# Kernel optimization log

Hardware: AMD Instinct MI355X
Metric: run time of the kernel (lower is better)

The kernel has to match this reference:

```python
import jax, jax.numpy as jnp
import numpy as np

B, S, DIM, H, DH, FF = 2, 2048, 2048, 16, 128, 8192
EPS = 1e-6


def rmsnorm(x, g):
    xf = x.astype(jnp.float32)
    y = xf * jax.lax.rsqrt(jnp.mean(xf * xf, axis=-1, keepdims=True) + EPS)
    return y.astype(x.dtype) * g


def rope_cache(seq_len, head_dim):
    inv_freq = 1.0 / (10000.0 ** (jnp.arange(0, head_dim, 2, dtype=jnp.float32) / head_dim))
    t = jnp.arange(seq_len, dtype=jnp.float32)
    freqs = jnp.outer(t, inv_freq)              # [S, DH/2]
    emb = jnp.concatenate([freqs, freqs], -1)   # [S, DH]
    return jnp.cos(emb), jnp.sin(emb)


def rotate_half(x):
    x1, x2 = jnp.split(x, 2, axis=-1)
    return jnp.concatenate([-x2, x1], axis=-1)


def apply_rope(x, cos, sin):
    # x: [B,H,S,DH]; cos/sin: [S,DH] broadcast per position
    c = cos[None, None, :, :]
    s = sin[None, None, :, :]
    return x * c + rotate_half(x) * s


def setup_inputs() -> dict:
    key = jax.random.key(0)
    ks = jax.random.split(key, 10)
    std = 0.02
    x = jax.random.normal(ks[0], (B, S, DIM), jnp.float32)
    mask = jnp.tril(jnp.ones((S, S), dtype=bool))[None, None]  # causal [1,1,S,S]
    wq = jax.random.normal(ks[1], (H * DH, DIM), jnp.float32) * std
    wk = jax.random.normal(ks[2], (H * DH, DIM), jnp.float32) * std
    wv = jax.random.normal(ks[3], (H * DH, DIM), jnp.float32) * std
    wo = jax.random.normal(ks[4], (DIM, H * DH), jnp.float32) * std
    w1 = jax.random.normal(ks[5], (FF, DIM), jnp.float32) * std
    w2 = jax.random.normal(ks[6], (DIM, FF), jnp.float32) * std
    w3 = jax.random.normal(ks[7], (FF, DIM), jnp.float32) * std
    g_attn = jnp.ones((DIM,), jnp.float32)
    g_ffn = jnp.ones((DIM,), jnp.float32)
    return {"x": x, "mask": mask, "wq": wq, "wk": wk, "wv": wv, "wo": wo,
            "w1": w1, "w2": w2, "w3": w3, "g_attn": g_attn, "g_ffn": g_ffn}


def reference(x, mask, wq, wk, wv, wo, w1, w2, w3, g_attn, g_ffn):
    b, s, _ = x.shape
    scale = 1.0 / np.sqrt(DH)
    # --- attention sublayer ---
    h = rmsnorm(x, g_attn)
    q = jnp.einsum('bsd,ed->bse', h, wq).reshape(b, s, H, DH).transpose(0, 2, 1, 3)
    k = jnp.einsum('bsd,ed->bse', h, wk).reshape(b, s, H, DH).transpose(0, 2, 1, 3)
    v = jnp.einsum('bsd,ed->bse', h, wv).reshape(b, s, H, DH).transpose(0, 2, 1, 3)
    cos, sin = rope_cache(s, DH)
    q = apply_rope(q, cos, sin)
    k = apply_rope(k, cos, sin)
    scores = jnp.einsum('bhqd,bhkd->bhqk', q, k) * scale
    scores = jnp.where(mask, scores, -1e9)
    attn = jax.nn.softmax(scores, axis=-1)
    o = jnp.einsum('bhqk,bhkd->bhqd', attn, v)
    o = o.transpose(0, 2, 1, 3).reshape(b, s, H * DH)
    x = x + jnp.einsum('bse,de->bsd', o, wo)
    # --- SwiGLU FFN sublayer ---
    h2 = rmsnorm(x, g_ffn)
    u = jnp.einsum('bsd,fd->bsf', h2, w1)
    g = jnp.einsum('bsd,fd->bsf', h2, w3)
    ff = jnp.einsum('bsf,df->bsd', jax.nn.silu(u) * g, w2)
    return x + ff
```

## Files before the change

kernel.cpp:

```cpp
#include <hip/hip_runtime.h>
#include <hip/hip_bf16.h>
#include <math.h>

typedef __hip_bfloat16 bf16;
typedef short short8 __attribute__((ext_vector_type(8)));
typedef float f32x4 __attribute__((ext_vector_type(4)));

#define Bq 2
#define Sq 2048
#define Dq 2048
#define Hq 16
#define DHq 128
#define FFq 8192
#define Mq 4096

__device__ __forceinline__ float b2f(bf16 x) { return __bfloat162float(x); }
__device__ __forceinline__ bf16 f2b(float x) { return __float2bfloat16(x); }

__device__ __forceinline__ void gload16(const void* g, void* lds_base) {
  __builtin_amdgcn_global_load_lds(
      (const __attribute__((address_space(1))) void*)g,
      (__attribute__((address_space(3))) void*)lds_base,
      16, 0, 0);
}

__global__ __launch_bounds__(256)
void conv_k(const float* __restrict__ src, bf16* __restrict__ dst, long n) {
  const long stride = (long)gridDim.x * 256 * 8;
  for (long i = ((long)blockIdx.x * 256 + threadIdx.x) * 8; i < n; i += stride) {
    f32x4 a = *(const f32x4*)(src + i);
    f32x4 b = *(const f32x4*)(src + i + 4);
    union { short8 s; bf16 h[8]; } u;
#pragma unroll
    for (int j = 0; j < 4; ++j) { u.h[j] = f2b(a[j]); u.h[j + 4] = f2b(b[j]); }
    *(short8*)(dst + i) = u.s;
  }
}

#define BAR8() { asm volatile("" ::: "memory"); __builtin_amdgcn_s_barrier(); asm volatile("" ::: "memory"); }
#define VMC4() { asm volatile("s_waitcnt vmcnt(4)" ::: "memory"); __builtin_amdgcn_sched_barrier(0); }
#define VMC2() { asm volatile("s_waitcnt vmcnt(2)" ::: "memory"); __builtin_amdgcn_sched_barrier(0); }

#define STG8(Gp, ldX, rowOff, kt, XsBuf)                                        \
  gload16(Gp + (size_t)((rowOff) + w8 + lr) * (size_t)(ldX) + (kt) + sCol,      \
          &XsBuf[(rowOff) + w8][0]);                                            \
  gload16(Gp + (size_t)((rowOff) + 64 + w8 + lr) * (size_t)(ldX) + (kt) + sCol, \
          &XsBuf[(rowOff) + 64 + w8][0]);

#define RD_A8(dst, XsBuf, mb)                                                   \
  _Pragma("unroll") for (int mi = 0; mi < 4; ++mi) {                            \
    const int ra = wmBase + ((mb) + mi) * 16 + c;                               \
    _Pragma("unroll") for (int kk = 0; kk < 2; ++kk)                            \
      dst[mi][kk] = *(const short8*)&XsBuf[ra][(((kk * 4 + g) ^ (ra & 7)) << 3)]; \
  }

#define RD_B8(dst, XsBuf, nb_)                                                  \
  _Pragma("unroll") for (int ni = 0; ni < 2; ++ni) {                            \
    const int rb = wnBase + ((nb_) + ni) * 16 + c;                              \
    _Pragma("unroll") for (int kk = 0; kk < 2; ++kk)                            \
      dst[ni][kk] = *(const short8*)&XsBuf[rb][(((kk * 4 + g) ^ (rb & 7)) << 3)]; \
  }

#define MFMA_Q8(afv, bfv, mb, nb_)                                              \
  __builtin_amdgcn_s_setprio(1);                                                \
  _Pragma("unroll") for (int mi = 0; mi < 4; ++mi)                              \
    _Pragma("unroll") for (int ni = 0; ni < 2; ++ni)                            \
      _Pragma("unroll") for (int kk = 0; kk < 2; ++kk)                          \
        acc[(mb) + mi][(nb_) + ni] = __builtin_amdgcn_mfma_f32_16x16x32_bf16(   \
            afv[mi][kk], bfv[ni][kk], acc[(mb) + mi][(nb_) + ni], 0, 0, 0);     \
  __builtin_amdgcn_s_setprio(0);

template <int EPI>
__global__ __launch_bounds__(512, 2)
void gemm8(const bf16* __restrict__ A, const bf16* __restrict__ Bt,
           const void* __restrict__ R, void* __restrict__ C,
           int N, int K, int ldb, long long boff) {
  __shared__ __align__(16) bf16 As[2][256][64];
  __shared__ __align__(16) bf16 Bs[2][256][64];
  const int tid = threadIdx.x;
  const int w = tid >> 6, l = tid & 63;
  const int g = l >> 4, c = l & 15;
  const int w8 = w * 8, lr = l >> 3;
  const int sCol = (((l & 7) ^ lr) << 3);

  const int nwg = gridDim.x * gridDim.y;
  const int orig = blockIdx.x + blockIdx.y * gridDim.x;
  const int qq = nwg >> 3, rr8 = nwg & 7;
  const int xcd = orig & 7, idx8 = orig >> 3;
  const int wg = (xcd < rr8 ? xcd * (qq + 1) : rr8 * (qq + 1) + (xcd - rr8) * qq) + idx8;
  const int bm = (wg / gridDim.x) * 256;
  const int bn = (wg % gridDim.x) * 256;

  const int wmBase = (w >> 2) * 128;
  const int wnBase = (w & 3) * 64;

  const bf16* Ab = A + (size_t)bm * K;
  const bf16* Bb = Bt + (size_t)bn * ldb + (size_t)boff;

  f32x4 acc[8][4] = {};
  const int nt = K >> 6;

  STG8(Ab, K, 0, 0, As[0]); STG8(Ab, K, 128, 0, As[0]);
  STG8(Bb, ldb, 0, 0, Bs[0]); STG8(Bb, ldb, 128, 0, Bs[0]);
  STG8(Bb, ldb, 0, 64, Bs[1]); STG8(Bb, ldb, 128, 64, Bs[1]);
  VMC4(); BAR8();

  short8 af[4][2], af2[4][2], bf[2][2], bf2[2][2];
  for (int it = 0; it < (nt >> 1); ++it) {
    const int t = it * 2;
    const int kt1 = (t + 1) << 6;
    const int kt2 = (t + 2 < nt ? t + 2 : nt - 1) << 6;
    const int kt3 = (t + 3 < nt ? t + 3 : nt - 1) << 6;
    RD_A8(af, As[0], 0); RD_B8(bf, Bs[0], 0); RD_B8(bf2, Bs[0], 2);
    STG8(Ab, K, 0, kt1, As[1]); STG8(Ab, K, 128, kt1, As[1]);
    MFMA_Q8(af, bf, 0, 0); MFMA_Q8(af, bf2, 0, 2);
    BAR8();
    RD_A8(af2, As[0], 4);
    STG8(Bb, ldb, 0, kt2, Bs[0]); STG8(Bb, ldb, 128, kt2, Bs[0]);
    MFMA_Q8(af2, bf, 4, 0); MFMA_Q8(af2, bf2, 4, 2);
    VMC4(); BAR8();
    RD_A8(af, As[1], 0); RD_B8(bf, Bs[1], 0); RD_B8(bf2, Bs[1], 2);
    STG8(Ab, K, 0, kt2, As[0]); STG8(Ab, K, 128, kt2, As[0]);
    MFMA_Q8(af, bf, 0, 0); MFMA_Q8(af, bf2, 0, 2);
    BAR8();
    RD_A8(af2, As[1], 4);
    STG8(Bb, ldb, 0, kt3, Bs[1]); STG8(Bb, ldb, 128, kt3, Bs[1]);
    MFMA_Q8(af2, bf, 4, 0); MFMA_Q8(af2, bf2, 4, 2);
    VMC4(); BAR8();
  }

  const int rbase = bm + wmBase + g * 4;
  const int cbase = bn + wnBase + c;
#pragma unroll
  for (int m = 0; m < 8; ++m)
#pragma unroll
    for (int r = 0; r < 4; ++r) {
      const int row = rbase + m * 16 + r;
#pragma unroll
      for (int n = 0; n < 4; ++n) {
        const size_t idx = (size_t)row * N + (cbase + n * 16);
        float vacc = acc[m][n][r];
        if (EPI == 1) {
          ((float*)C)[idx] = vacc + ((const float*)R)[idx];
        } else if (EPI == 2) {
          const float u = b2f(((const bf16*)R)[idx]);
          ((bf16*)C)[idx] = f2b((u / (1.f + expf(-u))) * vacc);
        } else {
          ((bf16*)C)[idx] = f2b(vacc);
        }
      }
    }
}

#define RD_A12(dst, XsBuf)                                                      \
  _Pragma("unroll") for (int mi = 0; mi < 4; ++mi) {                            \
    const int ra = wmB12 + mi * 16 + c;                                         \
    _Pragma("unroll") for (int kk = 0; kk < 2; ++kk)                            \
      dst[mi][kk] = *(const short8*)&XsBuf[ra][(((kk * 4 + g) ^ (ra & 7)) << 3)]; \
  }

#define RD_B12(dst, XsBuf, nb_)                                                 \
  _Pragma("unroll") for (int ni = 0; ni < 2; ++ni) {                            \
    const int rb = wnB12 + ((nb_) + ni) * 16 + c;                               \
    _Pragma("unroll") for (int kk = 0; kk < 2; ++kk)                            \
      dst[ni][kk] = *(const short8*)&XsBuf[rb][(((kk * 4 + g) ^ (rb & 7)) << 3)]; \
  }

#define MFMA_H12(afv, bfv, nb_)                                                 \
  __builtin_amdgcn_s_setprio(1);                                                \
  _Pragma("unroll") for (int mi = 0; mi < 4; ++mi)                              \
    _Pragma("unroll") for (int ni = 0; ni < 2; ++ni)                            \
      _Pragma("unroll") for (int kk = 0; kk < 2; ++kk)                          \
        acc[mi][(nb_) + ni] = __builtin_amdgcn_mfma_f32_16x16x32_bf16(          \
            afv[mi][kk], bfv[ni][kk], acc[mi][(nb_) + ni], 0, 0, 0);            \
  __builtin_amdgcn_s_setprio(0);

template <int EPI>
__global__ __launch_bounds__(512, 2)
void gemm12(const bf16* __restrict__ A, const bf16* __restrict__ Bt,
            const void* __restrict__ R, void* __restrict__ C,
            int N, int K, int ldb, long long boff) {
  __shared__ __align__(16) bf16 As[2][128][64];
  __shared__ __align__(16) bf16 Bs[2][256][64];
  const int tid = threadIdx.x;
  const int w = tid >> 6, l = tid & 63;
  const int g = l >> 4, c = l & 15;
  const int w8 = w * 8, lr = l >> 3;
  const int sCol = (((l & 7) ^ lr) << 3);

  const int nwg = gridDim.x * gridDim.y;
  const int orig = blockIdx.x + blockIdx.y * gridDim.x;
  const int qq = nwg >> 3, rr8 = nwg & 7;
  const int xcd = orig & 7, idx8 = orig >> 3;
  const int wg = (xcd < rr8 ? xcd * (qq + 1) : rr8 * (qq + 1) + (xcd - rr8) * qq) + idx8;
  const int bm = (wg / gridDim.x) * 128;
  const int bn = (wg % gridDim.x) * 256;

  const int wmB12 = (w >> 2) * 64;
  const int wnB12 = (w & 3) * 64;

  const bf16* Ab = A + (size_t)bm * K;
  const bf16* Bb = Bt + (size_t)bn * ldb + (size_t)boff;

  f32x4 acc[4][4] = {};
  const int nt = K >> 6;

  STG8(Ab, K, 0, 0, As[0]);
  STG8(Bb, ldb, 0, 0, Bs[0]); STG8(Bb, ldb, 128, 0, Bs[0]);
  STG8(Ab, K, 0, 64, As[1]);
  VMC2(); BAR8();

  short8 af[4][2], af2[4][2], bfa[2][2], bfa2[2][2], bfb[2][2], bfb2[2][2];
  for (int it = 0; it < (nt >> 1); ++it) {
    const int t = it * 2;
    const int kt1 = (t + 1) << 6;
    const int kt2 = (t + 2 < nt ? t + 2 : nt - 1) << 6;
    const int kt3 = (t + 3 < nt ? t + 3 : nt - 1) << 6;
    RD_A12(af, As[0]); RD_B12(bfa, Bs[0], 0);
    STG8(Bb, ldb, 0, kt1, Bs[1]); STG8(Bb, ldb, 128, kt1, Bs[1]);
    MFMA_H12(af, bfa, 0);
    BAR8();
    RD_B12(bfa2, Bs[0], 2);
    STG8(Ab, K, 0, kt2, As[0]);
    MFMA_H12(af, bfa2, 2);
    VMC2(); BAR8();
    RD_A12(af2, As[1]); RD_B12(bfb, Bs[1], 0);
    STG8(Bb, ldb, 0, kt2, Bs[0]); STG8(Bb, ldb, 128, kt2, Bs[0]);
    MFMA_H12(af2, bfb, 0);
    BAR8();
    RD_B12(bfb2, Bs[1], 2);
    STG8(Ab, K, 0, kt3, As[1]);
    MFMA_H12(af2, bfb2, 2);
    VMC2(); BAR8();
  }

  const int rbase = bm + wmB12 + g * 4;
  const int cbase = bn + wnB12 + c;
#pragma unroll
  for (int m = 0; m < 4; ++m)
#pragma unroll
    for (int r = 0; r < 4; ++r) {
      const int row = rbase + m * 16 + r;
#pragma unroll
      for (int n = 0; n < 4; ++n) {
        const size_t idx = (size_t)row * N + (cbase + n * 16);
        float vacc = acc[m][n][r];
        if (EPI == 1) {
          ((float*)C)[idx] = vacc + ((const float*)R)[idx];
        } else if (EPI == 2) {
          const float u = b2f(((const bf16*)R)[idx]);
          ((bf16*)C)[idx] = f2b((u / (1.f + expf(-u))) * vacc);
        } else {
          ((bf16*)C)[idx] = f2b(vacc);
        }
      }
    }
}

template <int EPI>
__global__ __launch_bounds__(256)
void gemm2(const bf16* __restrict__ A, const float* __restrict__ Bt,
           const void* __restrict__ R, void* __restrict__ C,
           int N, int K, int ldb, long long boff) {
  __shared__ __align__(16) bf16 As[128][64];
  __shared__ __align__(16) float Bsf[128][64];
  const int tid = threadIdx.x;
  const int w = tid >> 6;
  const int l = tid & 63;

  const int nwg = gridDim.x * gridDim.y;
  const int orig = blockIdx.x + blockIdx.y * gridDim.x;
  const int qq = nwg >> 3, rr8 = nwg & 7;
  const int xcd = orig & 7, idx8 = orig >> 3;
  const int wg = (xcd < rr8 ? xcd * (qq + 1) : rr8 * (qq + 1) + (xcd - rr8) * qq) + idx8;
  const int bm = (wg / gridDim.x) * 128;
  const int bn = (wg % gridDim.x) * 128;

  const int wr = (w >> 1) * 64;
  const int wc = (w & 1) * 64;
  f32x4 acc[4][4] = {};

  const bf16* Ab = A + (size_t)bm * K;
  const float* Bb = Bt + (size_t)bn * ldb + (size_t)boff;

  const int aSrcCol = (((l & 7) ^ (l >> 3)) << 3);
  const int bKey = (w * 4 + (l >> 4)) & 7;
  const int bSrcCol = (((l & 15) ^ bKey) << 2);

  for (int kt = 0; kt < K; kt += 64) {
    __syncthreads();
#pragma unroll
    for (int i = 0; i < 4; ++i)
      gload16(Ab + (size_t)(i * 32 + w * 8 + (l >> 3)) * K + kt + aSrcCol,
              &As[i * 32 + w * 8][0]);
#pragma unroll
    for (int i = 0; i < 8; ++i)
      gload16(Bb + (size_t)(i * 16 + w * 4 + (l >> 4)) * ldb + kt + bSrcCol,
              &Bsf[i * 16 + w * 4][0]);
    __syncthreads();

#pragma unroll
    for (int kk = 0; kk < 2; ++kk) {
      short8 af[4], bfv[4];
#pragma unroll
      for (int m = 0; m < 4; ++m) {
        const int ra = wr + m * 16 + (l & 15);
        const int pb = (kk * 4 + (l >> 4)) ^ (ra & 7);
        af[m] = *(const short8*)&As[ra][pb * 8];
      }
#pragma unroll
      for (int n = 0; n < 4; ++n) {
        const int rb = wc + n * 16 + (l & 15);
        const int b0 = kk * 8 + (l >> 4) * 2;
        const f32x4 x0 = *(const f32x4*)&Bsf[rb][(b0 ^ (rb & 7)) * 4];
        const f32x4 x1 = *(const f32x4*)&Bsf[rb][((b0 + 1) ^ (rb & 7)) * 4];
        union { short8 s; bf16 h[8]; } u;
#pragma unroll
        for (int j = 0; j < 4; ++j) { u.h[j] = f2b(x0[j]); u.h[j + 4] = f2b(x1[j]); }
        bfv[n] = u.s;
      }
#pragma unroll
      for (int m = 0; m < 4; ++m)
#pragma unroll
        for (int n = 0; n < 4; ++n)
          acc[m][n] = __builtin_amdgcn_mfma_f32_16x16x32_bf16(af[m], bfv[n], acc[m][n], 0, 0, 0);
    }
  }

  const int rbase = bm + wr + (l >> 4) * 4;
  const int cbase = bn + wc + (l & 15);
#pragma unroll
  for (int m = 0; m < 4; ++m)
#pragma unroll
    for (int r = 0; r < 4; ++r) {
      const int row = rbase + m * 16 + r;
#pragma unroll
      for (int n = 0; n < 4; ++n) {
        const size_t idx = (size_t)row * N + (cbase + n * 16);
        float vacc = acc[m][n][r];
        if (EPI == 1) {
          ((float*)C)[idx] = vacc + ((const float*)R)[idx];
        } else if (EPI == 2) {
          const float u = b2f(((const bf16*)R)[idx]);
          ((bf16*)C)[idx] = f2b((u / (1.f + expf(-u))) * vacc);
        } else {
          ((bf16*)C)[idx] = f2b(vacc);
        }
      }
    }
}

__global__ __launch_bounds__(256)
void rmsnorm_k(const float* __restrict__ xin, const float* __restrict__ g,
               bf16* __restrict__ out) {
  const int row = blockIdx.x;
  const int tid = threadIdx.x;
  const float* xp = xin + (size_t)row * Dq + tid * 8;
  f32x4 a = *(const f32x4*)xp, b = *(const f32x4*)(xp + 4);
  float xf[8];
#pragma unroll
  for (int j = 0; j < 4; ++j) { xf[j] = a[j]; xf[j + 4] = b[j]; }
  float ss = 0.f;
#pragma unroll
  for (int j = 0; j < 8; ++j) ss += xf[j] * xf[j];
#pragma unroll
  for (int off = 32; off > 0; off >>= 1) ss += __shfl_down(ss, off);
  __shared__ float red[4];
  if ((tid & 63) == 0) red[tid >> 6] = ss;
  __syncthreads();
  const float rms = rsqrtf((red[0] + red[1] + red[2] + red[3]) * (1.f / (float)Dq) + 1e-6f);
  const float* gp = g + tid * 8;
  f32x4 ga = *(const f32x4*)gp, gb = *(const f32x4*)(gp + 4);
  union { short8 s; bf16 h[8]; } uo;
#pragma unroll
  for (int j = 0; j < 4; ++j) {
    uo.h[j] = f2b(xf[j] * rms * ga[j]);
    uo.h[j + 4] = f2b(xf[j + 4] * rms * gb[j]);
  }
  *(short8*)(out + (size_t)row * Dq + tid * 8) = uo.s;
}

__global__ __launch_bounds__(256)
void rope_k(bf16* __restrict__ q, bf16* __restrict__ k, int ld) {
  const size_t idx = (size_t)blockIdx.x * 256 + threadIdx.x;
  const int i = (int)(idx & 63);
  const int h = (int)((idx >> 6) & 15);
  const int s = (int)((idx >> 10) & 2047);
  const int b = (int)(idx >> 21);
  const float f = (float)s * powf(10000.f, -(float)i * (1.f / 64.f));
  float sn, cs;
  sincosf(f, &sn, &cs);
  const size_t base = ((size_t)(b * Sq + s)) * ld + h * DHq + i;
  const float qa = b2f(q[base]), qb_ = b2f(q[base + 64]);
  q[base] = f2b(qa * cs - qb_ * sn);
  q[base + 64] = f2b(qb_ * cs + qa * sn);
  const float ka = b2f(k[base]), kb_ = b2f(k[base + 64]);
  k[base] = f2b(ka * cs - kb_ * sn);
  k[base + 64] = f2b(kb_ * cs + ka * sn);
}

__device__ __forceinline__ int swz8(int row) { return (((row >> 3) ^ row) & 7) << 3; }

#define ATTN_COMPUTE(AQ, QB, QROW, M_, L_, OACC, KV0, CUR)                        \
  {                                                                               \
    f32x4 sc[4] = {};                                                             \
    __builtin_amdgcn_s_setprio(1);                                                \
    _Pragma("unroll") for (int n = 0; n < 4; ++n) {                               \
      const int krow = n * 16 + c;                                                \
      const int sw = swz8(krow);                                                  \
      _Pragma("unroll") for (int kk = 0; kk < 4; ++kk) {                          \
        short8 ak = *(const short8*)&Ks[CUR][krow][(kk * 32 + g * 8) ^ sw];       \
        sc[n] = __builtin_amdgcn_mfma_f32_16x16x32_bf16(ak, AQ[kk], sc[n], 0, 0, 0); \
      }                                                                           \
    }                                                                             \
    __builtin_amdgcn_s_setprio(0);                                                \
    float p[4][4];                                                                \
    float tmax = -3.0e38f;                                                        \
    if ((KV0) + 63 <= (QB)) {                                                     \
      _Pragma("unroll") for (int n = 0; n < 4; ++n)                               \
        _Pragma("unroll") for (int r = 0; r < 4; ++r) {                           \
          const float val = sc[n][r] * SCALE;                                     \
          p[n][r] = val;                                                          \
          tmax = fmaxf(tmax, val);                                                \
        }                                                                         \
    } else {                                                                      \
      _Pragma("unroll") for (int n = 0; n < 4; ++n)                               \
        _Pragma("unroll") for (int r = 0; r < 4; ++r) {                           \
          const int kvg = (KV0) + n * 16 + g * 4 + r;                             \
          float val = sc[n][r] * SCALE;                                           \
          if (kvg > (QROW)) val = -3.0e38f;                                       \
          p[n][r] = val;                                                          \
          tmax = fmaxf(tmax, val);                                                \
        }                                                                         \
    }                                                                             \
    tmax = fmaxf(tmax, __shfl_xor(tmax, 16));                                     \
    tmax = fmaxf(tmax, __shfl_xor(tmax, 32));                                     \
    const bool grow = !__all(tmax <= M_);                                         \
    const float m_new = grow ? fmaxf(M_, tmax) : M_;                              \
    float tsum = 0.f;                                                             \
    _Pragma("unroll") for (int n = 0; n < 4; ++n)                                 \
      _Pragma("unroll") for (int r = 0; r < 4; ++r) {                             \
        const float pv = expf(p[n][r] - m_new);                                   \
        p[n][r] = pv;                                                             \
        tsum += pv;                                                               \
      }                                                                           \
    tsum += __shfl_xor(tsum, 16);                                                 \
    tsum += __shfl_xor(tsum, 32);                                                 \
    if (grow) {                                                                   \
      const float corr = expf(M_ - m_new);                                        \
      L_ = L_ * corr + tsum;                                                      \
      M_ = m_new;                                                                 \
      _Pragma("unroll") for (int dt = 0; dt < 8; ++dt) OACC[dt] *= corr;          \
    } else {                                                                      \
      L_ += tsum;                                                                 \
    }                                                                             \
    const int keyc = (c ^ (c >> 3)) & 7;                                          \
    _Pragma("unroll") for (int n = 0; n < 4; ++n) {                               \
      union { unsigned long long u; bf16 hh[4]; } pk;                             \
      _Pragma("unroll") for (int r = 0; r < 4; ++r) pk.hh[r] = f2b(p[n][r]);      \
      const int blk = (2 * n + (g >> 1)) ^ keyc;                                  \
      *(unsigned long long*)&Ps[w][c][blk * 8 + (g & 1) * 4] = pk.u;              \
    }                                                                             \
    short8 ap[2];                                                                 \
    _Pragma("unroll") for (int kk = 0; kk < 2; ++kk)                              \
      ap[kk] = *(const short8*)&Ps[w][c][(kk * 32 + g * 8) ^ (keyc << 3)];        \
    __builtin_amdgcn_s_setprio(1);                                                \
    _Pragma("unroll") for (int dt = 0; dt < 8; ++dt) {                            \
      const int vrow = dt * 16 + c;                                               \
      const int vsw = swz8(vrow);                                                 \
      _Pragma("unroll") for (int kk = 0; kk < 2; ++kk) {                          \
        short8 av = *(const short8*)&Vt[CUR][vrow][(kk * 32 + g * 8) ^ vsw];      \
        OACC[dt] = __builtin_amdgcn_mfma_f32_16x16x32_bf16(av, ap[kk], OACC[dt], 0, 0, 0); \
      }                                                                           \
    }                                                                             \
    __builtin_amdgcn_s_setprio(0);                                                \
  }

__global__ __launch_bounds__(512)
void attn_k(const bf16* __restrict__ q, const bf16* __restrict__ k,
            const bf16* __restrict__ v, bf16* __restrict__ o, int ld) {
  __shared__ __align__(16) bf16 Ks[2][64][128];
  __shared__ __align__(16) bf16 Vt[2][128][64];
  __shared__ __align__(16) bf16 Ps[8][16][64];
  const int tid = threadIdx.x;
  const int w = tid >> 6, l = tid & 63;
  const int g = l >> 4, c = l & 15;
  const int x = blockIdx.x;
  const int h = blockIdx.y;
  const int b = blockIdx.z;
  const size_t hoff = (size_t)h * DHq;
  const float SCALE = 0.08838834764831845f;

  const int q0h = (15 - x) * 128, q0l = x * 128;
  const int qbh = q0h + w * 16, qbl = q0l + w * 16;
  const int qrh = qbh + c, qrl = qbl + c;

  short8 aqh[4], aql[4];
  {
    const bf16* qph = q + (size_t)(b * Sq + qrh) * ld + hoff + g * 8;
    const bf16* qpl = q + (size_t)(b * Sq + qrl) * ld + hoff + g * 8;
#pragma unroll
    for (int kk = 0; kk < 4; ++kk) {
      aqh[kk] = *(const short8*)(qph + kk * 32);
      aql[kk] = *(const short8*)(qpl + kk * 32);
    }
  }

  float mh = -3.0e38f, lh = 0.f, ml = -3.0e38f, ll_ = 0.f;
  f32x4 oh[8] = {}, ol[8] = {};

  const int stRow = tid >> 4;
  const int stBlk = tid & 15;
  const int ntiles = (q0h >> 6) + 2;

  {
#pragma unroll
    for (int i = 0; i < 2; ++i) {
      const int kr = i * 32 + w * 4 + (l >> 4);
      const int key = (kr ^ (kr >> 3)) & 7;
      gload16(k + (size_t)(b * Sq + kr) * ld + hoff + ((c ^ key) << 3),
              &Ks[0][i * 32 + w * 4][0]);
    }
    const int c0 = stBlk * 8;
#pragma unroll
    for (int i = 0; i < 2; ++i) {
      const int vr = i * 32 + stRow;
      union { short8 s; bf16 hh[8]; } uv;
      uv.s = *(const short8*)(v + (size_t)(b * Sq + vr) * ld + hoff + c0);
#pragma unroll
      for (int j = 0; j < 8; ++j) Vt[0][c0 + j][vr ^ swz8(c0 + j)] = uv.hh[j];
    }
  }
  __syncthreads();

  for (int t = 0; t < ntiles; ++t) {
    const int cur = t & 1, nxt = cur ^ 1;
    const int kv0 = t * 64;
    const bool pf = (t + 1 < ntiles);
    short8 vpa, vpb;
    if (pf) {
      const int kvn = kv0 + 64;
#pragma unroll
      for (int i = 0; i < 2; ++i) {
        const int kr = i * 32 + w * 4 + (l >> 4);
        const int key = (kr ^ (kr >> 3)) & 7;
        gload16(k + (size_t)(b * Sq + kvn + kr) * ld + hoff + ((c ^ key) << 3),
                &Ks[nxt][i * 32 + w * 4][0]);
      }
      vpa = *(const short8*)(v + (size_t)(b * Sq + kvn + stRow) * ld + hoff + stBlk * 8);
      vpb = *(const short8*)(v + (size_t)(b * Sq + kvn + 32 + stRow) * ld + hoff + stBlk * 8);
    }

    if (kv0 <= qbh + 15) ATTN_COMPUTE(aqh, qbh, qrh, mh, lh, oh, kv0, cur);

    if (pf) {
      const int c0 = stBlk * 8;
      union { short8 s; bf16 hh[8]; } uv;
      uv.s = vpa;
#pragma unroll
      for (int j = 0; j < 8; ++j) Vt[nxt][c0 + j][stRow ^ swz8(c0 + j)] = uv.hh[j];
      uv.s = vpb;
#pragma unroll
      for (int j = 0; j < 8; ++j) Vt[nxt][c0 + j][(32 + stRow) ^ swz8(c0 + j)] = uv.hh[j];
    }

    if (kv0 <= qbl + 15) ATTN_COMPUTE(aql, qbl, qrl, ml, ll_, ol, kv0, cur);

    __syncthreads();
  }

  {
    const float inv = 1.f / lh;
    bf16* op = o + (size_t)(b * Sq + qrh) * Dq + hoff + g * 4;
#pragma unroll
    for (int dt = 0; dt < 8; ++dt) {
      union { unsigned long long u; bf16 hh[4]; } pk;
#pragma unroll
      for (int r = 0; r < 4; ++r) pk.hh[r] = f2b(oh[dt][r] * inv);
      *(unsigned long long*)(op + dt * 16) = pk.u;
    }
  }
  {
    const float inv = 1.f / ll_;
    bf16* op = o + (size_t)(b * Sq + qrl) * Dq + hoff + g * 4;
#pragma unroll
    for (int dt = 0; dt < 8; ++dt) {
      union { unsigned long long u; bf16 hh[4]; } pk;
#pragma unroll
      for (int r = 0; r < 4; ++r) pk.hh[r] = f2b(ol[dt][r] * inv);
      *(unsigned long long*)(op + dt * 16) = pk.u;
    }
  }
}

extern "C" void kernel_launch(void* const* d_in, const int* in_sizes, int n_in,
                              void* d_out, int out_size, void* d_ws, size_t ws_size,
                              hipStream_t stream) {
  (void)in_sizes; (void)n_in; (void)out_size;
  const float* x  = (const float*)d_in[0];
  const float* wq = (const float*)d_in[2];
  const float* wk = (const float*)d_in[3];
  const float* wv = (const float*)d_in[4];
  const float* wo = (const float*)d_in[5];
  const float* w1 = (const float*)d_in[6];
  const float* w2 = (const float*)d_in[7];
  const float* w3 = (const float*)d_in[8];
  const float* ga = (const float*)d_in[9];
  const float* gf = (const float*)d_in[10];
  float* out = (float*)d_out;

  char* ws = (char*)d_ws;
  dim3 blk(256);
  dim3 gA(8, Hq, Bq);
  dim3 blkA(512);
  dim3 blk8(512);

  const size_t SZ_H   = (size_t)Mq * Dq * 2;
  const size_t SZ_QKV = (size_t)Mq * 3 * Dq * 2;
  const size_t SZ_W4  = (size_t)Dq * Dq * 2;
  const size_t SZ_W13 = (size_t)FFq * Dq * 2;
  const size_t ACT    = SZ_H + SZ_QKV;
  const size_t WTS    = 3 * SZ_W4 + SZ_W4 + 3 * SZ_W13;
  const size_t NEED   = ACT + WTS;

  if (ws_size >= NEED) {
    bf16* h    = (bf16*)(ws);
    bf16* qkv  = (bf16*)(ws + SZ_H);
    bf16* ob   = h;
    bf16* h2   = qkv;
    bf16* ub   = (bf16*)(ws + 2 * SZ_H);
    char* wb   = ws + ACT;
    bf16* wqkv_b = (bf16*)(wb);
    bf16* wo_b   = (bf16*)(wb + 3 * SZ_W4);
    bf16* w1_b   = (bf16*)(wb + 4 * SZ_W4);
    bf16* w3_b   = (bf16*)(wb + 4 * SZ_W4 + SZ_W13);
    bf16* w2_b   = (bf16*)(wb + 4 * SZ_W4 + 2 * SZ_W13);

    const long nW4 = (long)Dq * Dq, nW13 = (long)FFq * Dq;
    conv_k<<<1024, blk, 0, stream>>>(wq, wqkv_b, nW4);
    conv_k<<<1024, blk, 0, stream>>>(wk, wqkv_b + nW4, nW4);
    conv_k<<<1024, blk, 0, stream>>>(wv, wqkv_b + 2 * nW4, nW4);
    conv_k<<<1024, blk, 0, stream>>>(wo, wo_b, nW4);
    conv_k<<<2048, blk, 0, stream>>>(w1, w1_b, nW13);
    conv_k<<<2048, blk, 0, stream>>>(w3, w3_b, nW13);
    conv_k<<<2048, blk, 0, stream>>>(w2, w2_b, nW13);

    rmsnorm_k<<<Mq, blk, 0, stream>>>(x, ga, h);
    gemm12<0><<<dim3(24, 32), blk8, 0, stream>>>(h, wqkv_b, nullptr, qkv, 6144, Dq, Dq, 0);
    rope_k<<<(Bq * Sq * Hq * 64) / 256, blk, 0, stream>>>(qkv, qkv + Dq, 3 * Dq);
    attn_k<<<gA, blkA, 0, stream>>>(qkv, qkv + Dq, qkv + 2 * Dq, ob, 3 * Dq);
    gemm12<1><<<dim3(8, 32), blk8, 0, stream>>>(ob, wo_b, x, out, Dq, Dq, Dq, 0);
    rmsnorm_k<<<Mq, blk, 0, stream>>>(out, gf, h2);
    gemm8<0><<<dim3(32, 16), blk8, 0, stream>>>(h2, w1_b, nullptr, ub, FFq, Dq, Dq, 0);
    gemm8<2><<<dim3(32, 16), blk8, 0, stream>>>(h2, w3_b, ub, ub, FFq, Dq, Dq, 0);
    gemm12<1><<<dim3(8, 32), blk8, 0, stream>>>(ub, w2_b, out, out, Dq, FFq, FFq, 0);
  } else {
    const size_t MS = (size_t)Mq * Dq * 2;
    bf16* h  = (bf16*)(ws);
    bf16* kb = (bf16*)(ws + MS);
    bf16* vb = (bf16*)(ws + 2 * MS);
    bf16* qb = (bf16*)(ws + 3 * MS);
    bf16* ub = (bf16*)(ws);
    bf16* ob = h;
    bf16* h2 = qb;

    dim3 gD(Dq / 128, Mq / 128);
    dim3 gU(32, Mq / 128);
    dim3 gAB(Sq / 128, Hq, Bq);
    (void)gAB;

    rmsnorm_k<<<Mq, blk, 0, stream>>>(x, ga, h);
    gemm2<0><<<gD, blk, 0, stream>>>(h, wq, nullptr, qb, Dq, Dq, Dq, 0);
    gemm2<0><<<gD, blk, 0, stream>>>(h, wk, nullptr, kb, Dq, Dq, Dq, 0);
    gemm2<0><<<gD, blk, 0, stream>>>(h, wv, nullptr, vb, Dq, Dq, Dq, 0);
    rope_k<<<(Bq * Sq * Hq * 64) / 256, blk, 0, stream>>>(qb, kb, Dq);
    attn_k<<<gA, blkA, 0, stream>>>(qb, kb, vb, ob, Dq);
    gemm2<1><<<gD, blk, 0, stream>>>(ob, wo, x, out, Dq, Dq, Dq, 0);
    rmsnorm_k<<<Mq, blk, 0, stream>>>(out, gf, h2);
    for (int hh = 0; hh < 2; ++hh) {
      const long long bo13 = (long long)hh * 4096 * 2048;
      gemm2<0><<<gU, blk, 0, stream>>>(h2, w1, nullptr, ub, 4096, Dq, Dq, bo13);
      gemm2<2><<<gU, blk, 0, stream>>>(h2, w3, ub, ub, 4096, Dq, Dq, bo13);
      gemm2<1><<<gD, blk, 0, stream>>>(ub, w2, out, out, Dq, 4096, FFq,
                                       (long long)hh * 4096);
    }
  }
}
```

Baseline: 832.2 us.

## Switch gemm8 to 32x32x16 MFMA and remap tiles to XCDs by columns

Result: slower. 860.4 us (+3.4%).

```diff
diff --git a/kernel.cpp b/kernel.cpp
--- a/kernel.cpp
+++ b/kernel.cpp
@@ -5,6 +5,7 @@
 typedef __hip_bfloat16 bf16;
 typedef short short8 __attribute__((ext_vector_type(8)));
 typedef float f32x4 __attribute__((ext_vector_type(4)));
+typedef float f32x16 __attribute__((ext_vector_type(16)));
 
 #define Bq 2
 #define Sq 2048
@@ -47,27 +48,27 @@
   gload16(Gp + (size_t)((rowOff) + 64 + w8 + lr) * (size_t)(ldX) + (kt) + sCol, \
           &XsBuf[(rowOff) + 64 + w8][0]);
 
-#define RD_A8(dst, XsBuf, mb)                                                   \
-  _Pragma("unroll") for (int mi = 0; mi < 4; ++mi) {                            \
-    const int ra = wmBase + ((mb) + mi) * 16 + c;                               \
-    _Pragma("unroll") for (int kk = 0; kk < 2; ++kk)                            \
-      dst[mi][kk] = *(const short8*)&XsBuf[ra][(((kk * 4 + g) ^ (ra & 7)) << 3)]; \
-  }
-
-#define RD_B8(dst, XsBuf, nb_)                                                  \
+#define RD_A32(dst, XsBuf, mb)                                                  \
+  _Pragma("unroll") for (int mi = 0; mi < 2; ++mi) {                            \
+    const int ra = wmBase + ((mb) + mi) * 32 + (l & 31);                        \
+    _Pragma("unroll") for (int ks = 0; ks < 4; ++ks)                            \
+      dst[mi][ks] = *(const short8*)&XsBuf[ra][(((ks * 2 + g5) ^ (ra & 7)) << 3)]; \
+  }
+
+#define RD_B32(dst, XsBuf)                                                      \
   _Pragma("unroll") for (int ni = 0; ni < 2; ++ni) {                            \
-    const int rb = wnBase + ((nb_) + ni) * 16 + c;                              \
-    _Pragma("unroll") for (int kk = 0; kk < 2; ++kk)                            \
-      dst[ni][kk] = *(const short8*)&XsBuf[rb][(((kk * 4 + g) ^ (rb & 7)) << 3)]; \
-  }
-
-#define MFMA_Q8(afv, bfv, mb, nb_)                                              \
+    const int rb = wnBase + ni * 32 + (l & 31);                                 \
+    _Pragma("unroll") for (int ks = 0; ks < 4; ++ks)                            \
+      dst[ni][ks] = *(const short8*)&XsBuf[rb][(((ks * 2 + g5) ^ (rb & 7)) << 3)]; \
+  }
+
+#define MFMA32(afv, bfv, mb)                                                    \
   __builtin_amdgcn_s_setprio(1);                                                \
-  _Pragma("unroll") for (int mi = 0; mi < 4; ++mi)                              \
+  _Pragma("unroll") for (int mi = 0; mi < 2; ++mi)                              \
     _Pragma("unroll") for (int ni = 0; ni < 2; ++ni)                            \
-      _Pragma("unroll") for (int kk = 0; kk < 2; ++kk)                          \
-        acc[(mb) + mi][(nb_) + ni] = __builtin_amdgcn_mfma_f32_16x16x32_bf16(   \
-            afv[mi][kk], bfv[ni][kk], acc[(mb) + mi][(nb_) + ni], 0, 0, 0);     \
+      _Pragma("unroll") for (int ks = 0; ks < 4; ++ks)                          \
+        acc[(mb) + mi][ni] = __builtin_amdgcn_mfma_f32_32x32x16_bf16(           \
+            afv[mi][ks], bfv[ni][ks], acc[(mb) + mi][ni], 0, 0, 0);             \
   __builtin_amdgcn_s_setprio(0);
 
 template <int EPI>
@@ -79,17 +80,14 @@
   __shared__ __align__(16) bf16 Bs[2][256][64];
   const int tid = threadIdx.x;
   const int w = tid >> 6, l = tid & 63;
-  const int g = l >> 4, c = l & 15;
+  const int g5 = l >> 5;
   const int w8 = w * 8, lr = l >> 3;
   const int sCol = (((l & 7) ^ lr) << 3);
 
-  const int nwg = gridDim.x * gridDim.y;
   const int orig = blockIdx.x + blockIdx.y * gridDim.x;
-  const int qq = nwg >> 3, rr8 = nwg & 7;
   const int xcd = orig & 7, idx8 = orig >> 3;
-  const int wg = (xcd < rr8 ? xcd * (qq + 1) : rr8 * (qq + 1) + (xcd - rr8) * qq) + idx8;
-  const int bm = (wg / gridDim.x) * 256;
-  const int bn = (wg % gridDim.x) * 256;
+  const int bn = (xcd * 4 + (idx8 & 3)) * 256;
+  const int bm = (idx8 >> 2) * 256;
 
   const int wmBase = (w >> 2) * 128;
   const int wnBase = (w & 3) * 64;
@@ -97,7 +95,7 @@
   const bf16* Ab = A + (size_t)bm * K;
   const bf16* Bb = Bt + (size_t)bn * ldb + (size_t)boff;
 
-  f32x4 acc[8][4] = {};
+  f32x16 acc[4][2] = {};
   const int nt = K >> 6;
 
   STG8(Ab, K, 0, 0, As[0]); STG8(Ab, K, 128, 0, As[0]);
@@ -105,41 +103,40 @@
   STG8(Bb, ldb, 0, 64, Bs[1]); STG8(Bb, ldb, 128, 64, Bs[1]);
   VMC4(); BAR8();
 
-  short8 af[4][2], af2[4][2], bf[2][2], bf2[2][2];
+  short8 af[2][4], af2[2][4], bf[2][4];
   for (int it = 0; it < (nt >> 1); ++it) {
     const int t = it * 2;
     const int kt1 = (t + 1) << 6;
     const int kt2 = (t + 2 < nt ? t + 2 : nt - 1) << 6;
     const int kt3 = (t + 3 < nt ? t + 3 : nt - 1) << 6;
-    RD_A8(af, As[0], 0); RD_B8(bf, Bs[0], 0); RD_B8(bf2, Bs[0], 2);
+    RD_A32(af, As[0], 0); RD_B32(bf, Bs[0]);
     STG8(Ab, K, 0, kt1, As[1]); STG8(Ab, K, 128, kt1, As[1]);
-    MFMA_Q8(af, bf, 0, 0); MFMA_Q8(af, bf2, 0, 2);
+    MFMA32(af, bf, 0);
     BAR8();
-    RD_A8(af2, As[0], 4);
+    RD_A32(af2, As[0], 2);
     STG8(Bb, ldb, 0, kt2, Bs[0]); STG8(Bb, ldb, 128, kt2, Bs[0]);
-    MFMA_Q8(af2, bf, 4, 0); MFMA_Q8(af2, bf2, 4, 2);
+    MFMA32(af2, bf, 2);
     VMC4(); BAR8();
-    RD_A8(af, As[1], 0); RD_B8(bf, Bs[1], 0); RD_B8(bf2, Bs[1], 2);
+    RD_A32(af, As[1], 0); RD_B32(bf, Bs[1]);
     STG8(Ab, K, 0, kt2, As[0]); STG8(Ab, K, 128, kt2, As[0]);
-    MFMA_Q8(af, bf, 0, 0); MFMA_Q8(af, bf2, 0, 2);
+    MFMA32(af, bf, 0);
     BAR8();
-    RD_A8(af2, As[1], 4);
+    RD_A32(af2, As[1], 2);
     STG8(Bb, ldb, 0, kt3, Bs[1]); STG8(Bb, ldb, 128, kt3, Bs[1]);
-    MFMA_Q8(af2, bf, 4, 0); MFMA_Q8(af2, bf2, 4, 2);
+    MFMA32(af2, bf, 2);
     VMC4(); BAR8();
   }
 
-  const int rbase = bm + wmBase + g * 4;
-  const int cbase = bn + wnBase + c;
-#pragma unroll
-  for (int m = 0; m < 8; ++m)
-#pragma unroll
-    for (int r = 0; r < 4; ++r) {
-      const int row = rbase + m * 16 + r;
-#pragma unroll
-      for (int n = 0; n < 4; ++n) {
-        const size_t idx = (size_t)row * N + (cbase + n * 16);
-        float vacc = acc[m][n][r];
+  const int cbase = bn + wnBase + (l & 31);
+#pragma unroll
+  for (int m = 0; m < 4; ++m)
+#pragma unroll
+    for (int reg = 0; reg < 16; ++reg) {
+      const int row = bm + wmBase + m * 32 + (reg & 3) + 8 * (reg >> 2) + 4 * g5;
+#pragma unroll
+      for (int n = 0; n < 2; ++n) {
+        const size_t idx = (size_t)row * N + (cbase + n * 32);
+        float vacc = acc[m][n][reg];
         if (EPI == 1) {
           ((float*)C)[idx] = vacc + ((const float*)R)[idx];
         } else if (EPI == 2) {
@@ -666,8 +663,6 @@
 
     dim3 gD(Dq / 128, Mq / 128);
     dim3 gU(32, Mq / 128);
-    dim3 gAB(Sq / 128, Hq, Bq);
-    (void)gAB;
 
     rmsnorm_k<<<Mq, blk, 0, stream>>>(x, ga, h);
     gemm2<0><<<gD, blk, 0, stream>>>(h, wq, nullptr, qb, Dq, Dq, Dq, 0);
```
